# Performance work log

Measured on AMD Instinct MI355X. Metric: run time of the kernel, lower is better.

## Reference

```python
import jax, jax.numpy as jnp
import numpy as np

N_NODES = 100000
N_EDGES = 1_600_000
F_IN = 128
N_HEADS = 4
F_OUT = 32


def setup_inputs() -> dict:
    key = jax.random.key(0)
    k1, k2, k3, k4, k5 = jax.random.split(key, 5)
    h_in = jax.random.normal(k1, (N_NODES, F_IN), dtype=jnp.float32)
    edge_index = jax.random.randint(k2, (2, N_EDGES), 0, N_NODES, dtype=jnp.int64)
    # Xavier-uniform-ish scales
    W = jax.random.normal(k3, (F_IN, N_HEADS * F_OUT), dtype=jnp.float32) * (1.0 / np.sqrt(F_IN))
    b = jnp.zeros((N_HEADS * F_OUT,), dtype=jnp.float32)
    a_src = jax.random.normal(k4, (N_HEADS, F_OUT), dtype=jnp.float32) * 0.1
    a_tgt = jax.random.normal(k5, (N_HEADS, F_OUT), dtype=jnp.float32) * 0.1
    return {"h_in": h_in, "edge_index": edge_index, "W": W, "b": b, "a_src": a_src, "a_tgt": a_tgt}


def reference(h_in, edge_index, W, b, a_src, a_tgt):
    # Eval mode: dropout is identity.
    src, tgt = edge_index[0], edge_index[1]
    # Shared linear projection: [N, H, F]
    h_proj = (h_in @ W + b).reshape(-1, N_HEADS, F_OUT)
    # Per-node attention score contributions: [N, H]
    score_src = jnp.einsum('nhf,hf->nh', h_proj, a_src)
    score_tgt = jnp.einsum('nhf,hf->nh', h_proj, a_tgt)
    # Edge-level scores (gather), LeakyReLU(0.2) as in the original: [E, H]
    e = jax.nn.leaky_relu(score_tgt[tgt] + score_src[src], negative_slope=0.2)
    # Segment softmax over incoming edges of each target node.
    # (Original uses raw exp without max subtraction; replicate faithfully.)
    exp_e = jnp.exp(e)
    denom = jax.ops.segment_sum(exp_e, tgt, num_segments=N_NODES)  # [N, H]
    alpha = exp_e / (denom[tgt] + 1e-16)                            # [E, H]
    # Weighted message aggregation: [N, H, F]
    msg = alpha[:, :, None] * h_proj[src]                           # [E, H, F]
    h_new = jax.ops.segment_sum(msg, tgt, num_segments=N_NODES)
    # concat=True branch: original computes activation(new_features) but returns
    # the UN-activated concatenated view (new_features_sigm is unused) -> replicate.
    return h_new.reshape(N_NODES, N_HEADS * F_OUT)
```

## Files before the change

kernel.cpp:

```cpp
#include <hip/hip_runtime.h>
#include <hip/hip_bf16.h>

typedef unsigned short u16;
typedef unsigned int u32;
typedef long long i64;
typedef __attribute__((ext_vector_type(8))) short s8v;
typedef __attribute__((ext_vector_type(4))) float f32x4;

#define SUBCAP 1023
#define BKT_CAP (8 * SUBCAP)

__device__ __forceinline__ float bf2f(u16 u) {
    union { u32 i; float f; } x; x.i = ((u32)u) << 16; return x.f;
}
__device__ __forceinline__ u16 f2bf(float f) {
    union { float f; u32 i; } x; x.f = f;
    u32 v = x.i;
    u32 r = v + 0x7FFFu + ((v >> 16) & 1u);
    return (u16)(r >> 16);
}
__device__ __forceinline__ int get_i(const void* p, size_t i, int m64) {
    return m64 ? (int)((const i64*)p)[i] : ((const int*)p)[i];
}
__device__ __forceinline__ float lrelu_clamp(float v) {
    v = v > 0.f ? v : 0.2f * v;
    return fminf(v, 80.f);
}

__global__ __launch_bounds__(256) void k_init(
    const u16* __restrict__ hin, const int* __restrict__ eidx, int* __restrict__ flags,
    const u16* __restrict__ W, u16* __restrict__ Wt, int* __restrict__ bucket_cnt, int ncnt)
{
    const int b = blockIdx.x, t = threadIdx.x;
    if (b == 0) {
        __shared__ int c1, c2;
        if (t == 0) { c1 = 0; c2 = 0; }
        __syncthreads();
        int l1 = 0, l2 = 0;
        for (int i = t; i < 8192; i += 256) {
            float v = bf2f(hin[i]);
            if (!(fabsf(v) <= 100.f)) l1++;
            if ((i & 1) && eidx[i] == 0) l2++;
        }
        atomicAdd(&c1, l1); atomicAdd(&c2, l2);
        __syncthreads();
        if (t == 0) {
            flags[0] = (c1 > 40) ? 1 : 0;
            flags[1] = (c2 > 3000) ? 1 : 0;
        }
    } else {
        int i = (b - 1) * 256 + t;
        int k = i >> 7, n = i & 127;
        Wt[(size_t)n * 128 + k] = W[(size_t)k * 128 + n];
    }
    for (int i = b * 256 + t; i < ncnt; i += gridDim.x * 256) bucket_cnt[i] = 0;
}

__global__ __launch_bounds__(256) void k_bktA(
    const void* __restrict__ eidx, const int* __restrict__ flags,
    int* __restrict__ bucket_cnt, u32* __restrict__ bkt,
    int n_edges, int n_nodes, int nbk)
{
    __shared__ int2 ed[4096];
    __shared__ int lcnt[512];
    __shared__ int lpos[512];
    const int t = threadIdx.x;
    const int e0 = blockIdx.x * 4096;
    const int rep = blockIdx.x & 7;
    const int m64 = flags[1];
    const int nloc = min(4096, n_edges - e0);

    for (int i = t; i < 512; i += 256) lcnt[i] = 0;
    __syncthreads();

    for (int r = 0; r < 16; r++) {
        int i = r * 256 + t;
        if (i < nloc) {
            int e = e0 + i;
            int s  = get_i(eidx, e, m64);
            int tg = get_i(eidx, (size_t)n_edges + e, m64);
            s  = min(max(s, 0), n_nodes - 1);
            tg = min(max(tg, 0), n_nodes - 1);
            ed[i] = make_int2(s, tg);
            atomicAdd(&lcnt[tg >> 8], 1);
        }
    }
    __syncthreads();

    for (int bb = t; bb < nbk; bb += 256) {
        int c = lcnt[bb];
        lpos[bb] = c ? atomicAdd(&bucket_cnt[rep * 512 + bb], c) : 0;
    }
    __syncthreads();

    for (int r = 0; r < 16; r++) {
        int i = r * 256 + t;
        if (i < nloc) {
            int2 st = ed[i];
            int bb = st.y >> 8;
            int p = atomicAdd(&lpos[bb], 1);
            p = min(p, SUBCAP - 1);
            bkt[(size_t)bb * BKT_CAP + rep * SUBCAP + p] =
                ((u32)st.x << 8) | (u32)(st.y & 255);
        }
    }
}

__global__ __launch_bounds__(256) void k_bsort(
    const int* __restrict__ bucket_cnt, const u32* __restrict__ bkt,
    int* __restrict__ offs, int* __restrict__ src_sorted,
    int n_edges, int n_nodes, int nbk)
{
    __shared__ int s_a[512], s_b[512];
    __shared__ int tcnt[256], tpos[256];
    __shared__ int subcnt[8];
    __shared__ int Gb_sh, cntb_sh, total_sh;
    const int t = threadIdx.x;
    const int b = blockIdx.x;

    for (int i = t; i < 512; i += 256) {
        int tot = 0;
        if (i < nbk) {
            #pragma unroll
            for (int r = 0; r < 8; r++) tot += min(bucket_cnt[r * 512 + i], SUBCAP);
        }
        s_a[i] = tot;
    }
    if (t < 8) subcnt[t] = min(bucket_cnt[t * 512 + b], SUBCAP);
    __syncthreads();

    int* pa = s_a; int* pb = s_b;
    for (int off = 1; off < 512; off <<= 1) {
        #pragma unroll
        for (int k = 0; k < 2; k++) {
            int i = t + k * 256;
            pb[i] = pa[i] + (i >= off ? pa[i - off] : 0);
        }
        __syncthreads();
        int* sw = pa; pa = pb; pb = sw;
    }
    if (t == 0) {
        int run = 0;
        #pragma unroll
        for (int r = 0; r < 8; r++) run += subcnt[r];
        cntb_sh = run;
        Gb_sh = pa[b] - run;
        total_sh = pa[511];
    }
    __syncthreads();
    const int Gb = Gb_sh, total = total_sh;

    tcnt[t] = 0;
    __syncthreads();
    const u32* mybkt = bkt + (size_t)b * BKT_CAP;
    #pragma unroll
    for (int r = 0; r < 8; r++) {
        const int c = subcnt[r];
        const u32* sub = mybkt + r * SUBCAP;
        for (int i = t; i < c; i += 256)
            atomicAdd(&tcnt[sub[i] & 255], 1);
    }
    __syncthreads();

    int own = tcnt[t];
    s_a[t] = own;
    __syncthreads();
    for (int off = 1; off < 256; off <<= 1) {
        int x = (t >= off) ? s_a[t - off] : 0;
        __syncthreads();
        s_a[t] += x;
        __syncthreads();
    }
    const int texcl = s_a[t] - own;

    const int tgt_id = b * 256 + t;
    if (tgt_id < n_nodes) offs[tgt_id] = Gb + texcl;
    if (b == 0 && t == 0) offs[n_nodes] = total;
    tpos[t] = Gb + texcl;
    __syncthreads();
    #pragma unroll
    for (int r = 0; r < 8; r++) {
        const int c = subcnt[r];
        const u32* sub = mybkt + r * SUBCAP;
        for (int i = t; i < c; i += 256) {
            u32 v = sub[i];
            int p = atomicAdd(&tpos[v & 255], 1);
            src_sorted[p] = (int)(v >> 8);
        }
    }
}

__global__ __launch_bounds__(256) void k_proj_mfma(
    const u16* __restrict__ hin, const u16* __restrict__ Wt,
    const u16* __restrict__ bias, const u16* __restrict__ a_src,
    const u16* __restrict__ a_tgt, const int* __restrict__ flags,
    u16* __restrict__ hp, float* __restrict__ ssrc, float* __restrict__ stgt,
    int M)
{
    if (flags[0]) return;
    const int wave = threadIdx.x >> 6;
    const int lane = threadIdx.x & 63;
    const int q = lane >> 4, col = lane & 15;
    const int row0 = blockIdx.x * 64 + wave * 16;
    if (row0 >= M) return;

    const int arow = min(row0 + col, M - 1);
    f32x4 acc[8];
    #pragma unroll
    for (int ct = 0; ct < 8; ct++) acc[ct] = (f32x4){0.f, 0.f, 0.f, 0.f};

    #pragma unroll
    for (int kc = 0; kc < 4; kc++) {
        s8v afrag = *(const s8v*)(hin + (size_t)arow * 128 + kc * 32 + q * 8);
        #pragma unroll
        for (int ct = 0; ct < 8; ct++) {
            s8v bfrag = *(const s8v*)(Wt + (size_t)(ct * 16 + col) * 128 + kc * 32 + q * 8);
            acc[ct] = __builtin_amdgcn_mfma_f32_16x16x32_bf16(afrag, bfrag, acc[ct], 0, 0, 0);
        }
    }

    float bb[8], as[8], at[8];
    #pragma unroll
    for (int ct = 0; ct < 8; ct++) {
        int c = ct * 16 + col;
        bb[ct] = bf2f(bias[c]);
        as[ct] = bf2f(a_src[c]);
        at[ct] = bf2f(a_tgt[c]);
    }

    #pragma unroll
    for (int r = 0; r < 4; r++) {
        int row = row0 + q * 4 + r;
        float ps0 = 0.f, ps1 = 0.f, ps2 = 0.f, ps3 = 0.f;
        float pt0 = 0.f, pt1 = 0.f, pt2 = 0.f, pt3 = 0.f;
        float ov[8];
        #pragma unroll
        for (int ct = 0; ct < 8; ct++) {
            float v = acc[ct][r] + bb[ct];
            ov[ct] = v;
            float s = v * as[ct], t2 = v * at[ct];
            if (ct < 2)      { ps0 += s; pt0 += t2; }
            else if (ct < 4) { ps1 += s; pt1 += t2; }
            else if (ct < 6) { ps2 += s; pt2 += t2; }
            else             { ps3 += s; pt3 += t2; }
        }
        if (row < M) {
            union { ushort4 h[2]; uint4 qv; } pk;
            pk.h[0] = make_ushort4(f2bf(ov[0]), f2bf(ov[1]), f2bf(ov[2]), f2bf(ov[3]));
            pk.h[1] = make_ushort4(f2bf(ov[4]), f2bf(ov[5]), f2bf(ov[6]), f2bf(ov[7]));
            *(uint4*)(hp + (size_t)row * 128 + col * 8) = pk.qv;
        }
        #pragma unroll
        for (int m = 1; m < 16; m <<= 1) {
            ps0 += __shfl_xor(ps0, m); ps1 += __shfl_xor(ps1, m);
            ps2 += __shfl_xor(ps2, m); ps3 += __shfl_xor(ps3, m);
            pt0 += __shfl_xor(pt0, m); pt1 += __shfl_xor(pt1, m);
            pt2 += __shfl_xor(pt2, m); pt3 += __shfl_xor(pt3, m);
        }
        if (row < M && col < 4) {
            float vs = col == 0 ? ps0 : col == 1 ? ps1 : col == 2 ? ps2 : ps3;
            float vt = col == 0 ? pt0 : col == 1 ? pt1 : col == 2 ? pt2 : pt3;
            ssrc[(size_t)row * 4 + col] = vs;
            stgt[(size_t)row * 4 + col] = vt;
        }
    }
}

__global__ __launch_bounds__(256) void k_proj_f32(
    const float* __restrict__ hin, const float* __restrict__ W,
    const float* __restrict__ bias, const float* __restrict__ a_src,
    const float* __restrict__ a_tgt, const int* __restrict__ flags,
    u16* __restrict__ hp, float* __restrict__ ssrc, float* __restrict__ stgt,
    int n_nodes)
{
    if (!flags[0]) return;
    __shared__ u16 sh_hp[64][128];
    __shared__ float sh_s[64][4], sh_t[64][4];
    const int t = threadIdx.x;
    const int row0 = blockIdx.x * 64;
    const int cg = (t & 31) * 4;
    const int rg = (t >> 5) * 8;

    const float* hr[8];
    #pragma unroll
    for (int i = 0; i < 8; i++)
        hr[i] = hin + (size_t)min(row0 + rg + i, n_nodes - 1) * 128;

    float acc[8][4] = {};
    for (int k = 0; k < 128; k += 4) {
        float4 w0 = *(const float4*)(W + (size_t)(k + 0) * 128 + cg);
        float4 w1 = *(const float4*)(W + (size_t)(k + 1) * 128 + cg);
        float4 w2 = *(const float4*)(W + (size_t)(k + 2) * 128 + cg);
        float4 w3 = *(const float4*)(W + (size_t)(k + 3) * 128 + cg);
        #pragma unroll
        for (int i = 0; i < 8; i++) {
            float4 h4 = *(const float4*)(hr[i] + k);
            acc[i][0] += h4.x * w0.x + h4.y * w1.x + h4.z * w2.x + h4.w * w3.x;
            acc[i][1] += h4.x * w0.y + h4.y * w1.y + h4.z * w2.y + h4.w * w3.y;
            acc[i][2] += h4.x * w0.z + h4.y * w1.z + h4.z * w2.z + h4.w * w3.z;
            acc[i][3] += h4.x * w0.w + h4.y * w1.w + h4.z * w2.w + h4.w * w3.w;
        }
    }

    const float b0 = bias[cg], b1 = bias[cg + 1], b2 = bias[cg + 2], b3 = bias[cg + 3];
    const float as0 = a_src[cg], as1 = a_src[cg + 1], as2 = a_src[cg + 2], as3 = a_src[cg + 3];
    const float at0 = a_tgt[cg], at1 = a_tgt[cg + 1], at2 = a_tgt[cg + 2], at3 = a_tgt[cg + 3];
    const int head = (t & 31) >> 3;

    #pragma unroll
    for (int i = 0; i < 8; i++) {
        float v0 = acc[i][0] + b0, v1 = acc[i][1] + b1;
        float v2 = acc[i][2] + b2, v3 = acc[i][3] + b3;
        float p1 = v0 * as0 + v1 * as1 + v2 * as2 + v3 * as3;
        float p2 = v0 * at0 + v1 * at1 + v2 * at2 + v3 * at3;
        #pragma unroll
        for (int m = 1; m < 8; m <<= 1) {
            p1 += __shfl_xor(p1, m);
            p2 += __shfl_xor(p2, m);
        }
        if ((t & 7) == 0) { sh_s[rg + i][head] = p1; sh_t[rg + i][head] = p2; }
        int f0 = cg;
        sh_hp[rg + i][((f0 + 0) & 15) * 8 + ((f0 + 0) >> 4)] = f2bf(v0);
        sh_hp[rg + i][((f0 + 1) & 15) * 8 + ((f0 + 1) >> 4)] = f2bf(v1);
        sh_hp[rg + i][((f0 + 2) & 15) * 8 + ((f0 + 2) >> 4)] = f2bf(v2);
        sh_hp[rg + i][((f0 + 3) & 15) * 8 + ((f0 + 3) >> 4)] = f2bf(v3);
    }
    __syncthreads();

    for (int c = t; c < 1024; c += 256) {
        int r = c >> 4, off = (c & 15) * 8;
        int row = row0 + r;
        if (row < n_nodes)
            *(uint4*)(hp + (size_t)row * 128 + off) = *(const uint4*)&sh_hp[r][off];
    }
    {
        int r = t >> 2, h = t & 3;
        int row = row0 + r;
        if (row < n_nodes) {
            ssrc[(size_t)row * 4 + h] = sh_s[r][h];
            stgt[(size_t)row * 4 + h] = sh_t[r][h];
        }
    }
}

__global__ __launch_bounds__(256) void k_agg_csr(
    const int* __restrict__ offs, const int* __restrict__ src_sorted,
    const float* __restrict__ ssrc, const float* __restrict__ stgt,
    const void* __restrict__ hp, void* __restrict__ out,
    const int* __restrict__ flags, int n_nodes)
{
    __shared__ u16 ob[4][128];
    __shared__ float obf[4][128];
    const int wave = threadIdx.x >> 6;
    int wid = (blockIdx.x * 256 + threadIdx.x) >> 6;
    wid = min(wid, n_nodes - 1);
    const int lane = threadIdx.x & 63;
    const int fp32 = flags[0];
    const int d0 = offs[wid], d1 = offs[wid + 1];

    const int sub = lane >> 4;
    const int li = lane & 15;
    const u16* hpb = (const u16*)hp;
    const float4* ssrc4 = (const float4*)ssrc;
    const float4 st4 = ((const float4*)stgt)[wid];
    const int deg = d1 - d0;

    float a[8] = {};
    auto accum = [&](float4 w, uint4 v) {
        a[0] += w.x * bf2f((u16)(v.x & 0xffff));
        a[1] += w.x * bf2f((u16)(v.x >> 16));
        a[2] += w.y * bf2f((u16)(v.y & 0xffff));
        a[3] += w.y * bf2f((u16)(v.y >> 16));
        a[4] += w.z * bf2f((u16)(v.z & 0xffff));
        a[5] += w.z * bf2f((u16)(v.z >> 16));
        a[6] += w.w * bf2f((u16)(v.w & 0xffff));
        a[7] += w.w * bf2f((u16)(v.w >> 16));
    };

    const int nh = min(deg, 64);
    int my_s = 0;
    float4 my_w = make_float4(0.f, 0.f, 0.f, 0.f);
    if (nh > 0) {
        my_s = src_sorted[d0 + min(lane, nh - 1)];
        float4 cs = ssrc4[my_s];
        if (lane < nh) {
            my_w = make_float4(__expf(lrelu_clamp(cs.x + st4.x)),
                               __expf(lrelu_clamp(cs.y + st4.y)),
                               __expf(lrelu_clamp(cs.z + st4.z)),
                               __expf(lrelu_clamp(cs.w + st4.w)));
        }
    }

    const int ns = (nh + 3) >> 2;
    auto sload = [&](int k, uint4& vv) {
        if (k < ns) {
            int s = __shfl(my_s, k * 4 + sub);
            vv = *(const uint4*)(hpb + (size_t)s * 128 + li * 8);
        }
    };
    auto sacc = [&](int k, uint4 vv) {
        if (k < ns) {
            int idx = k * 4 + sub;
            float4 w;
            w.x = __shfl(my_w.x, idx);
            w.y = __shfl(my_w.y, idx);
            w.z = __shfl(my_w.z, idx);
            w.w = __shfl(my_w.w, idx);
            accum(w, vv);
        }
    };
    uint4 v0{}, v1{}, v2{}, v3{}, v4{}, v5{}, v6{}, v7{};
    sload(0, v0); sload(1, v1); sload(2, v2); sload(3, v3);
    sload(4, v4); sload(5, v5); sload(6, v6); sload(7, v7);
    sacc(0, v0); sload(8, v0);
    sacc(1, v1); sload(9, v1);
    sacc(2, v2); sload(10, v2);
    sacc(3, v3); sload(11, v3);
    sacc(4, v4); sload(12, v4);
    sacc(5, v5); sload(13, v5);
    sacc(6, v6); sload(14, v6);
    sacc(7, v7); sload(15, v7);
    sacc(8, v0); sacc(9, v1); sacc(10, v2); sacc(11, v3);
    sacc(12, v4); sacc(13, v5); sacc(14, v6); sacc(15, v7);

    float4 es_t = make_float4(0.f, 0.f, 0.f, 0.f);
    if (deg > 64) {
        for (int e = d0 + 64; e < d1; e += 4) {
            int idx = e + sub;
            int ok = idx < d1;
            int s = src_sorted[ok ? idx : d1 - 1];
            uint4 v = *(const uint4*)(hpb + (size_t)s * 128 + li * 8);
            float4 cs = ssrc4[s];
            float4 w = make_float4(__expf(lrelu_clamp(cs.x + st4.x)),
                                   __expf(lrelu_clamp(cs.y + st4.y)),
                                   __expf(lrelu_clamp(cs.z + st4.z)),
                                   __expf(lrelu_clamp(cs.w + st4.w)));
            if (!ok) w = make_float4(0.f, 0.f, 0.f, 0.f);
            accum(w, v);
            es_t.x += w.x; es_t.y += w.y; es_t.z += w.z; es_t.w += w.w;
        }
    }

    float4 es = my_w;
    #pragma unroll
    for (int m = 1; m < 16; m <<= 1) {
        es.x += __shfl_xor(es.x, m);
        es.y += __shfl_xor(es.y, m);
        es.z += __shfl_xor(es.z, m);
        es.w += __shfl_xor(es.w, m);
    }
    es.x += es_t.x; es.y += es_t.y; es.z += es_t.z; es.w += es_t.w;

    #pragma unroll
    for (int m = 0; m < 8; m++) {
        a[m] += __shfl_xor(a[m], 16);
        a[m] += __shfl_xor(a[m], 32);
    }
    es.x += __shfl_xor(es.x, 16); es.x += __shfl_xor(es.x, 32);
    es.y += __shfl_xor(es.y, 16); es.y += __shfl_xor(es.y, 32);
    es.z += __shfl_xor(es.z, 16); es.z += __shfl_xor(es.z, 32);
    es.w += __shfl_xor(es.w, 16); es.w += __shfl_xor(es.w, 32);

    float inv4[4] = {1.f / (es.x + 1e-16f), 1.f / (es.y + 1e-16f),
                     1.f / (es.z + 1e-16f), 1.f / (es.w + 1e-16f)};

    if (!fp32) {
        if (sub == 0) {
            #pragma unroll
            for (int m = 0; m < 8; m++)
                ob[wave][m * 16 + li] = f2bf(a[m] * inv4[m >> 1]);
        }
        __syncthreads();
        if (sub == 0) {
            uint4 ov = *(const uint4*)&ob[wave][li * 8];
            *(uint4*)((u16*)out + (size_t)wid * 128 + li * 8) = ov;
        }
    } else {
        if (sub == 0) {
            #pragma unroll
            for (int m = 0; m < 8; m++)
                obf[wave][m * 16 + li] = a[m] * inv4[m >> 1];
        }
        __syncthreads();
        float* of = (float*)out + (size_t)wid * 128;
        *(float2*)(of + lane * 2) = make_float2(obf[wave][lane * 2],
                                                obf[wave][lane * 2 + 1]);
    }
}

extern "C" void kernel_launch(void* const* d_in, const int* in_sizes, int n_in,
                              void* d_out, int out_size, void* d_ws, size_t ws_size,
                              hipStream_t stream)
{
    const void* h_in  = d_in[0];
    const void* eidx  = d_in[1];
    const void* W     = d_in[2];
    const void* bias  = d_in[3];
    const void* a_src = d_in[4];
    const void* a_tgt = d_in[5];

    const int n_nodes = in_sizes[0] / 128;
    const int n_edges = in_sizes[1] / 2;
    const int nbk = (n_nodes + 255) >> 8;
    const int nba = (n_edges + 4095) / 4096;

    char* p = (char*)d_ws;
    auto alloc = [&](size_t bytes) { char* q = p; p += (bytes + 255) & ~(size_t)255; return q; };
    int*   flags      = (int*)  alloc(256);
    void*  hp         = (void*) alloc((size_t)n_nodes * 128 * sizeof(float));
    u16*   Wt         = (u16*)  alloc(128 * 128 * sizeof(u16));
    float* ssrc       = (float*)alloc((size_t)n_nodes * 4 * sizeof(float));
    float* stgt       = (float*)alloc((size_t)n_nodes * 4 * sizeof(float));
    int*   offs       = (int*)  alloc(((size_t)n_nodes + 1) * sizeof(int));
    int*   bucket_cnt = (int*)  alloc(8 * 512 * sizeof(int));
    int*   src_sorted = (int*)  alloc((size_t)n_edges * sizeof(int));

    size_t bkt_bytes = (size_t)nbk * BKT_CAP * sizeof(u32);
    u32* bkt;
    if (bkt_bytes <= (size_t)n_nodes * 128 * 2)
        bkt = (u32*)((char*)hp + (size_t)n_nodes * 128 * 2);
    else
        bkt = (u32*)alloc(bkt_bytes);

    k_init     <<<65, 256, 0, stream>>>((const u16*)h_in, (const int*)eidx, flags,
                                        (const u16*)W, Wt, bucket_cnt, 8 * 512);
    k_bktA     <<<nba, 256, 0, stream>>>(eidx, flags, bucket_cnt, bkt,
                                         n_edges, n_nodes, nbk);
    k_bsort    <<<nbk, 256, 0, stream>>>(bucket_cnt, bkt, offs, src_sorted,
                                         n_edges, n_nodes, nbk);
    k_proj_mfma<<<(n_nodes + 63) / 64, 256, 0, stream>>>((const u16*)h_in, Wt, (const u16*)bias,
                                                         (const u16*)a_src, (const u16*)a_tgt,
                                                         flags, (u16*)hp, ssrc, stgt, n_nodes);
    k_proj_f32 <<<(n_nodes + 63) / 64, 256, 0, stream>>>((const float*)h_in, (const float*)W,
                                                         (const float*)bias, (const float*)a_src,
                                                         (const float*)a_tgt, flags, (u16*)hp,
                                                         ssrc, stgt, n_nodes);
    k_agg_csr  <<<(n_nodes + 3) / 4, 256, 0, stream>>>(offs, src_sorted, ssrc, stgt,
                                                       hp, d_out, flags, n_nodes);
}
```

Measured before the change: 328.4 us.

## Use split-bf16 MFMA for fp32 projection and fold attention vectors into W

The fp32 projection path switches from scalar FMA to MFMA. Inputs and W are split into bf16 hi/lo parts and three bf16 MFMAs are summed to approximate fp32 precision. The attention scores are computed directly from the fp32 input using W·a_src, W·a_tgt and bias·a products, which are precomputed in the init kernel. The aim is to move the projection GEMM onto the matrix cores, at the cost of a small precision loss from dropping the lo×lo term and extra init work.

```diff
diff --git a/kernel.cpp b/kernel.cpp
--- a/kernel.cpp
+++ b/kernel.cpp
@@ -29,7 +29,12 @@
 
 __global__ __launch_bounds__(256) void k_init(
     const u16* __restrict__ hin, const int* __restrict__ eidx, int* __restrict__ flags,
-    const u16* __restrict__ W, u16* __restrict__ Wt, int* __restrict__ bucket_cnt, int ncnt)
+    const u16* __restrict__ W, const float* __restrict__ Wf,
+    const float* __restrict__ biasf, const float* __restrict__ asrcf,
+    const float* __restrict__ atgtf,
+    u16* __restrict__ Wt, u16* __restrict__ Wt_hi, u16* __restrict__ Wt_lo,
+    float* __restrict__ wa, float* __restrict__ ba,
+    int* __restrict__ bucket_cnt, int ncnt)
 {
     const int b = blockIdx.x, t = threadIdx.x;
     if (b == 0) {
@@ -48,10 +53,34 @@
             flags[0] = (c1 > 40) ? 1 : 0;
             flags[1] = (c2 > 3000) ? 1 : 0;
         }
-    } else {
+    } else if (b <= 64) {
         int i = (b - 1) * 256 + t;
         int k = i >> 7, n = i & 127;
         Wt[(size_t)n * 128 + k] = W[(size_t)k * 128 + n];
+        float wf = Wf[(size_t)k * 128 + n];
+        u16 hi = f2bf(wf);
+        Wt_hi[(size_t)n * 128 + k] = hi;
+        Wt_lo[(size_t)n * 128 + k] = f2bf(wf - bf2f(hi));
+    } else if (b <= 68) {
+        int idx = (b - 65) * 256 + t;
+        int sel = idx >> 9, rem = idx & 511;
+        int h = rem >> 7, k = rem & 127;
+        const float* av = sel ? atgtf : asrcf;
+        float s = 0.f;
+        #pragma unroll 8
+        for (int f = 0; f < 32; f++)
+            s += Wf[(size_t)k * 128 + h * 32 + f] * av[h * 32 + f];
+        wa[idx] = s;
+    } else {
+        if (t < 8) {
+            int sel = t >> 2, h = t & 3;
+            const float* av = sel ? atgtf : asrcf;
+            float s = 0.f;
+            #pragma unroll 8
+            for (int f = 0; f < 32; f++)
+                s += biasf[h * 32 + f] * av[h * 32 + f];
+            ba[t] = s;
+        }
     }
     for (int i = b * 256 + t; i < ncnt; i += gridDim.x * 256) bucket_cnt[i] = 0;
 }
@@ -114,7 +143,7 @@
     __shared__ int s_a[512], s_b[512];
     __shared__ int tcnt[256], tpos[256];
     __shared__ int subcnt[8];
-    __shared__ int Gb_sh, cntb_sh, total_sh;
+    __shared__ int Gb_sh, total_sh;
     const int t = threadIdx.x;
     const int b = blockIdx.x;
 
@@ -143,7 +172,6 @@
         int run = 0;
         #pragma unroll
         for (int r = 0; r < 8; r++) run += subcnt[r];
-        cntb_sh = run;
         Gb_sh = pa[b] - run;
         total_sh = pa[511];
     }
@@ -198,10 +226,9 @@
     int M)
 {
     if (flags[0]) return;
-    const int wave = threadIdx.x >> 6;
     const int lane = threadIdx.x & 63;
     const int q = lane >> 4, col = lane & 15;
-    const int row0 = blockIdx.x * 64 + wave * 16;
+    const int row0 = blockIdx.x * 64 + (threadIdx.x >> 6) * 16;
     if (row0 >= M) return;
 
     const int arow = min(row0 + col, M - 1);
@@ -266,79 +293,94 @@
     }
 }
 
-__global__ __launch_bounds__(256) void k_proj_f32(
-    const float* __restrict__ hin, const float* __restrict__ W,
-    const float* __restrict__ bias, const float* __restrict__ a_src,
-    const float* __restrict__ a_tgt, const int* __restrict__ flags,
+__global__ __launch_bounds__(256) void k_proj_fm(
+    const float* __restrict__ hin, const u16* __restrict__ Wt_hi,
+    const u16* __restrict__ Wt_lo, const float* __restrict__ biasf,
+    const float* __restrict__ wa, const float* __restrict__ ba,
+    const int* __restrict__ flags,
     u16* __restrict__ hp, float* __restrict__ ssrc, float* __restrict__ stgt,
-    int n_nodes)
+    int M)
 {
     if (!flags[0]) return;
-    __shared__ u16 sh_hp[64][128];
-    __shared__ float sh_s[64][4], sh_t[64][4];
+    __shared__ float wal[1032];
     const int t = threadIdx.x;
-    const int row0 = blockIdx.x * 64;
-    const int cg = (t & 31) * 4;
-    const int rg = (t >> 5) * 8;
-
-    const float* hr[8];
-    #pragma unroll
-    for (int i = 0; i < 8; i++)
-        hr[i] = hin + (size_t)min(row0 + rg + i, n_nodes - 1) * 128;
-
-    float acc[8][4] = {};
-    for (int k = 0; k < 128; k += 4) {
-        float4 w0 = *(const float4*)(W + (size_t)(k + 0) * 128 + cg);
-        float4 w1 = *(const float4*)(W + (size_t)(k + 1) * 128 + cg);
-        float4 w2 = *(const float4*)(W + (size_t)(k + 2) * 128 + cg);
-        float4 w3 = *(const float4*)(W + (size_t)(k + 3) * 128 + cg);
-        #pragma unroll
-        for (int i = 0; i < 8; i++) {
-            float4 h4 = *(const float4*)(hr[i] + k);
-            acc[i][0] += h4.x * w0.x + h4.y * w1.x + h4.z * w2.x + h4.w * w3.x;
-            acc[i][1] += h4.x * w0.y + h4.y * w1.y + h4.z * w2.y + h4.w * w3.y;
-            acc[i][2] += h4.x * w0.z + h4.y * w1.z + h4.z * w2.z + h4.w * w3.z;
-            acc[i][3] += h4.x * w0.w + h4.y * w1.w + h4.z * w2.w + h4.w * w3.w;
-        }
-    }
-
-    const float b0 = bias[cg], b1 = bias[cg + 1], b2 = bias[cg + 2], b3 = bias[cg + 3];
-    const float as0 = a_src[cg], as1 = a_src[cg + 1], as2 = a_src[cg + 2], as3 = a_src[cg + 3];
-    const float at0 = a_tgt[cg], at1 = a_tgt[cg + 1], at2 = a_tgt[cg + 2], at3 = a_tgt[cg + 3];
-    const int head = (t & 31) >> 3;
-
-    #pragma unroll
-    for (int i = 0; i < 8; i++) {
-        float v0 = acc[i][0] + b0, v1 = acc[i][1] + b1;
-        float v2 = acc[i][2] + b2, v3 = acc[i][3] + b3;
-        float p1 = v0 * as0 + v1 * as1 + v2 * as2 + v3 * as3;
-        float p2 = v0 * at0 + v1 * at1 + v2 * at2 + v3 * at3;
-        #pragma unroll
-        for (int m = 1; m < 8; m <<= 1) {
-            p1 += __shfl_xor(p1, m);
-            p2 += __shfl_xor(p2, m);
-        }
-        if ((t & 7) == 0) { sh_s[rg + i][head] = p1; sh_t[rg + i][head] = p2; }
-        int f0 = cg;
-        sh_hp[rg + i][((f0 + 0) & 15) * 8 + ((f0 + 0) >> 4)] = f2bf(v0);
-        sh_hp[rg + i][((f0 + 1) & 15) * 8 + ((f0 + 1) >> 4)] = f2bf(v1);
-        sh_hp[rg + i][((f0 + 2) & 15) * 8 + ((f0 + 2) >> 4)] = f2bf(v2);
-        sh_hp[rg + i][((f0 + 3) & 15) * 8 + ((f0 + 3) >> 4)] = f2bf(v3);
-    }
-    __syncthreads();
-
-    for (int c = t; c < 1024; c += 256) {
-        int r = c >> 4, off = (c & 15) * 8;
-        int row = row0 + r;
-        if (row < n_nodes)
-            *(uint4*)(hp + (size_t)row * 128 + off) = *(const uint4*)&sh_hp[r][off];
-    }
-    {
-        int r = t >> 2, h = t & 3;
-        int row = row0 + r;
-        if (row < n_nodes) {
-            ssrc[(size_t)row * 4 + h] = sh_s[r][h];
-            stgt[(size_t)row * 4 + h] = sh_t[r][h];
+    for (int i = t; i < 1024; i += 256) wal[i] = wa[i];
+    if (t < 8) wal[1024 + t] = ba[t];
+    __syncthreads();
+
+    const int lane = t & 63;
+    const int q = lane >> 4, col = lane & 15;
+    const int row0 = blockIdx.x * 64 + (t >> 6) * 16;
+    if (row0 >= M) return;
+    const int arow = min(row0 + col, M - 1);
+
+    f32x4 acc[8];
+    #pragma unroll
+    for (int ct = 0; ct < 8; ct++) acc[ct] = (f32x4){0.f, 0.f, 0.f, 0.f};
+    float ps[4] = {0.f, 0.f, 0.f, 0.f}, pt[4] = {0.f, 0.f, 0.f, 0.f};
+
+    #pragma unroll
+    for (int kc = 0; kc < 4; kc++) {
+        const int ko = kc * 32 + q * 8;
+        const float* hrow = hin + (size_t)arow * 128 + ko;
+        float4 hva = *(const float4*)hrow;
+        float4 hvb = *(const float4*)(hrow + 4);
+        float hv[8] = {hva.x, hva.y, hva.z, hva.w, hvb.x, hvb.y, hvb.z, hvb.w};
+        s8v ahi, alo;
+        #pragma unroll
+        for (int j = 0; j < 8; j++) {
+            u16 hi = f2bf(hv[j]);
+            ahi[j] = (short)hi;
+            alo[j] = (short)f2bf(hv[j] - bf2f(hi));
+        }
+        #pragma unroll
+        for (int ct = 0; ct < 8; ct++) {
+            const size_t boff = (size_t)(ct * 16 + col) * 128 + ko;
+            s8v bhi = *(const s8v*)(Wt_hi + boff);
+            s8v blo = *(const s8v*)(Wt_lo + boff);
+            acc[ct] = __builtin_amdgcn_mfma_f32_16x16x32_bf16(ahi, bhi, acc[ct], 0, 0, 0);
+            acc[ct] = __builtin_amdgcn_mfma_f32_16x16x32_bf16(ahi, blo, acc[ct], 0, 0, 0);
+            acc[ct] = __builtin_amdgcn_mfma_f32_16x16x32_bf16(alo, bhi, acc[ct], 0, 0, 0);
+        }
+        #pragma unroll
+        for (int h = 0; h < 4; h++) {
+            float4 sa = *(const float4*)&wal[h * 128 + ko];
+            float4 sb = *(const float4*)&wal[h * 128 + ko + 4];
+            ps[h] += hv[0] * sa.x + hv[1] * sa.y + hv[2] * sa.z + hv[3] * sa.w
+                   + hv[4] * sb.x + hv[5] * sb.y + hv[6] * sb.z + hv[7] * sb.w;
+            float4 ta = *(const float4*)&wal[512 + h * 128 + ko];
+            float4 tb = *(const float4*)&wal[512 + h * 128 + ko + 4];
+            pt[h] += hv[0] * ta.x + hv[1] * ta.y + hv[2] * ta.z + hv[3] * ta.w
+                   + hv[4] * tb.x + hv[5] * tb.y + hv[6] * tb.z + hv[7] * tb.w;
+        }
+    }
+
+    #pragma unroll
+    for (int h = 0; h < 4; h++) {
+        ps[h] += __shfl_xor(ps[h], 16); ps[h] += __shfl_xor(ps[h], 32);
+        pt[h] += __shfl_xor(pt[h], 16); pt[h] += __shfl_xor(pt[h], 32);
+    }
+    if (q == 0 && row0 + col < M) {
+        #pragma unroll
+        for (int h = 0; h < 4; h++) {
+            ssrc[(size_t)(row0 + col) * 4 + h] = ps[h] + wal[1024 + h];
+            stgt[(size_t)(row0 + col) * 4 + h] = pt[h] + wal[1028 + h];
+        }
+    }
+
+    float bb[8];
+    #pragma unroll
+    for (int ct = 0; ct < 8; ct++) bb[ct] = biasf[ct * 16 + col];
+    #pragma unroll
+    for (int r = 0; r < 4; r++) {
+        int row = row0 + q * 4 + r;
+        if (row < M) {
+            union { ushort4 h[2]; uint4 qv; } pk;
+            pk.h[0] = make_ushort4(f2bf(acc[0][r] + bb[0]), f2bf(acc[1][r] + bb[1]),
+                                   f2bf(acc[2][r] + bb[2]), f2bf(acc[3][r] + bb[3]));
+            pk.h[1] = make_ushort4(f2bf(acc[4][r] + bb[4]), f2bf(acc[5][r] + bb[5]),
+                                   f2bf(acc[6][r] + bb[6]), f2bf(acc[7][r] + bb[7]));
+            *(uint4*)(hp + (size_t)row * 128 + col * 8) = pk.qv;
         }
     }
 }
@@ -509,6 +551,10 @@
     int*   flags      = (int*)  alloc(256);
     void*  hp         = (void*) alloc((size_t)n_nodes * 128 * sizeof(float));
     u16*   Wt         = (u16*)  alloc(128 * 128 * sizeof(u16));
+    u16*   Wt_hi      = (u16*)  alloc(128 * 128 * sizeof(u16));
+    u16*   Wt_lo      = (u16*)  alloc(128 * 128 * sizeof(u16));
+    float* wa         = (float*)alloc(1024 * sizeof(float));
+    float* ba         = (float*)alloc(8 * sizeof(float));
     float* ssrc       = (float*)alloc((size_t)n_nodes * 4 * sizeof(float));
     float* stgt       = (float*)alloc((size_t)n_nodes * 4 * sizeof(float));
     int*   offs       = (int*)  alloc(((size_t)n_nodes + 1) * sizeof(int));
@@ -522,8 +568,12 @@
     else
         bkt = (u32*)alloc(bkt_bytes);
 
-    k_init     <<<65, 256, 0, stream>>>((const u16*)h_in, (const int*)eidx, flags,
-                                        (const u16*)W, Wt, bucket_cnt, 8 * 512);
+    k_init     <<<70, 256, 0, stream>>>((const u16*)h_in, (const int*)eidx, flags,
+                                        (const u16*)W, (const float*)W,
+                                        (const float*)bias, (const float*)a_src,
+                                        (const float*)a_tgt,
+                                        Wt, Wt_hi, Wt_lo, wa, ba,
+                                        bucket_cnt, 8 * 512);
     k_bktA     <<<nba, 256, 0, stream>>>(eidx, flags, bucket_cnt, bkt,
                                          n_edges, n_nodes, nbk);
     k_bsort    <<<nbk, 256, 0, stream>>>(bucket_cnt, bkt, offs, src_sorted,
@@ -531,10 +581,9 @@
     k_proj_mfma<<<(n_nodes + 63) / 64, 256, 0, stream>>>((const u16*)h_in, Wt, (const u16*)bias,
                                                          (const u16*)a_src, (const u16*)a_tgt,
                                                          flags, (u16*)hp, ssrc, stgt, n_nodes);
-    k_proj_f32 <<<(n_nodes + 63) / 64, 256, 0, stream>>>((const float*)h_in, (const float*)W,
-                                                         (const float*)bias, (const float*)a_src,
-                                                         (const float*)a_tgt, flags, (u16*)hp,
-                                                         ssrc, stgt, n_nodes);
+    k_proj_fm  <<<(n_nodes + 63) / 64, 256, 0, stream>>>((const float*)h_in, Wt_hi, Wt_lo,
+                                                         (const float*)bias, wa, ba,
+                                                         flags, (u16*)hp, ssrc, stgt, n_nodes);
     k_agg_csr  <<<(n_nodes + 3) / 4, 256, 0, stream>>>(offs, src_sorted, ssrc, stgt,
                                                        hp, d_out, flags, n_nodes);
 }
```

Measured after the change: 307.9 us. 1.07x faster.
